# Kernel tuning notes

Hardware: AMD Instinct MI355X
Metric: run time of the kernel (lower is better)

The kernel has to match this reference:

```python
import jax, jax.numpy as jnp
import numpy as np

NORMALIZED_LENGTH = 512  # init kwarg
T_FRAMES = 32768
N_LM = 543  # mediapipe holistic landmark count


def setup_inputs() -> dict:
    key = jax.random.key(0)
    kf, kn, kd, ki = jax.random.split(key, 4)
    frames = jax.random.uniform(kf, (T_FRAMES, N_LM, 3), dtype=jnp.float32)
    nan_mask = jax.random.uniform(kn, (T_FRAMES, N_LM, 3)) < 0.10
    frames = jnp.where(nan_mask, jnp.float32(jnp.nan), frames)
    drop = jax.random.uniform(kd, (T_FRAMES,)) < 0.05
    hand_zone = jnp.arange(N_LM) >= 468
    frames = jnp.where(drop[:, None, None] & hand_zone[None, :, None], jnp.float32(jnp.nan), frames)
    lips_idx = jax.random.randint(ki, (40,), 0, 468, dtype=jnp.int32)
    return {"frames": frames, "lips_idx": lips_idx}


def _nan_mean0(x):
    # tf_nan_mean over axis 0 (keepdims); 0/0 -> NaN in TF is immediately zeroed
    # afterwards, so we emit 0 directly (identical forward values, safe grads).
    finite = ~jnp.isnan(x)
    s = jnp.where(finite, x, jnp.zeros((), x.dtype)).sum(axis=0, keepdims=True)
    c = finite.sum(axis=0, keepdims=True)
    return jnp.where(c == 0, jnp.zeros((), x.dtype), s / jnp.maximum(c, 1).astype(x.dtype))


def reference(frames, lips_idx):
    fr = frames[:, :, :2]                       # drop z coord
    lh = fr[:, 468:489]                         # [T, 21, 2]
    rh = fr[:, 522:543]                         # [T, 21, 2]
    lh = jnp.stack([lh[..., 0], 1.0 - lh[..., 1]], axis=-1)
    rh = jnp.stack([1.0 - rh[..., 0], 1.0 - rh[..., 1]], axis=-1)
    # stack hands, NaN->0, sum over the 2-hand axis
    hand = jnp.nan_to_num(lh) + jnp.nan_to_num(rh)   # [T, 21, 2]
    keep = hand.sum(axis=(1, 2)) != 0.0              # frames with >=1 visible hand
    hand = hand[keep]                                # [S, 21, 2]
    lips = fr[:, lips_idx][keep]                     # [S, 40, 2]
    lips = jnp.where(jnp.isnan(lips), _nan_mean0(lips), lips)
    raw = jnp.concatenate([hand, lips], axis=1)      # [S, 61, 2]
    S = int(raw.shape[0])
    # tf.linspace(0, S-1, L+1) cast to int32 -> segment boundaries (truncation)
    b = np.linspace(0.0, S - 1.0, NORMALIZED_LENGTH + 1).astype(np.int32)
    # frame t belongs to bin i with b[i] <= t < b[i+1]; t >= b[L] maps to L (dropped)
    seg = jnp.asarray(np.searchsorted(b, np.arange(S), side="right") - 1)
    sums = jax.ops.segment_sum(raw, seg, num_segments=NORMALIZED_LENGTH)
    cnt = jax.ops.segment_sum(jnp.ones((S,), raw.dtype), seg, num_segments=NORMALIZED_LENGTH)
    # raw is NaN-free at this point, so nan-mean == plain mean; empty bin -> NaN -> 0
    mean = jnp.where(cnt[:, None, None] == 0, jnp.zeros((), raw.dtype),
                     sums / jnp.maximum(cnt, 1.0)[:, None, None])
    sampled = mean.reshape(NORMALIZED_LENGTH, -1)    # Flatten -> [L, 122]
    rows = sampled.sum(axis=1) != 0.0                # drop all-zero (empty) bins
    return sampled[rows]
```

## Files before the change

kernel.cpp:

```cpp
#include <hip/hip_runtime.h>

#define T_FRAMES 32768
#define ROWF 1629
#define NSEG 512
#define NVAL 122
#define STRIDE 128

__global__ __launch_bounds__(256) void k1_keep_stats(
    const float* __restrict__ frames, const int* __restrict__ lips_idx,
    int* __restrict__ keep, float* __restrict__ lip_sum,
    int* __restrict__ lip_cnt, float* __restrict__ stage) {
  __shared__ float ls[80];
  __shared__ int lc[80];
  int tid = threadIdx.x;
  if (tid < 80) { ls[tid] = 0.0f; lc[tid] = 0; }
  __syncthreads();

  int lane = tid & 63;
  int wid = tid >> 6;
  int wpb = blockDim.x >> 6;
  int wpg = gridDim.x * wpb;

  for (int t = blockIdx.x * wpb + wid; t < T_FRAMES; t += wpg) {
    const float* f = frames + (size_t)t * ROWF;
    float* srow = stage + (size_t)t * STRIDE;

    float hv = 0.0f;
    if (lane < 42) {
      int j = lane >> 1, c = lane & 1;
      float lh = f[(468 + j) * 3 + c];
      float rh = f[(522 + j) * 3 + c];
      float a = (c == 0) ? lh : (1.0f - lh);
      float b = 1.0f - rh;
      a = (a == a) ? a : 0.0f;
      b = (b == b) ? b : 0.0f;
      hv = a + b;
      srow[lane] = hv;
    }
    float s = hv;
    #pragma unroll
    for (int off = 32; off > 0; off >>= 1) s += __shfl_down(s, off);
    s = __shfl(s, 0);
    int kp = (s != 0.0f) ? 1 : 0;
    if (lane == 0) keep[t] = kp;

    #pragma unroll
    for (int p = 0; p < 2; ++p) {
      int v = lane + p * 64;
      if (v < 80) {
        int j = v >> 1, c = v & 1;
        float x = f[lips_idx[j] * 3 + c];
        srow[42 + v] = x;
        if (kp && (x == x)) {
          atomicAdd(&ls[v], x);
          atomicAdd(&lc[v], 1);
        }
      }
    }
  }
  __syncthreads();
  if (tid < 80) {
    atomicAdd(&lip_sum[tid], ls[tid]);
    atomicAdd(&lip_cnt[tid], lc[tid]);
  }
}

__global__ __launch_bounds__(1024) void k2_scan(const int* __restrict__ keep,
                                                int* __restrict__ kept_t,
                                                int* __restrict__ Sp) {
  __shared__ int wsum[16];
  int tid = threadIdx.x;
  const int PER = T_FRAMES / 1024;
  int base = tid * PER;
  int fl[PER];
  int local = 0;
  #pragma unroll
  for (int k = 0; k < PER; ++k) { fl[k] = keep[base + k]; local += fl[k]; }

  int lane = tid & 63, wid = tid >> 6;
  int scan = local;
  #pragma unroll
  for (int off = 1; off < 64; off <<= 1) {
    int n = __shfl_up(scan, off);
    if (lane >= off) scan += n;
  }
  if (lane == 63) wsum[wid] = scan;
  __syncthreads();
  if (tid < 16) {
    int v = wsum[tid];
    #pragma unroll
    for (int off = 1; off < 16; off <<= 1) {
      int n = __shfl_up(v, off);
      if (tid >= off) v += n;
    }
    wsum[tid] = v;
  }
  __syncthreads();
  int excl = ((wid == 0) ? 0 : wsum[wid - 1]) + (scan - local);
  #pragma unroll
  for (int k = 0; k < PER; ++k) {
    if (fl[k]) kept_t[excl++] = base + k;
  }
  if (tid == 1023) Sp[0] = wsum[15];
}

__global__ __launch_bounds__(256) void k3_segments(
    const float* __restrict__ stage, const int* __restrict__ kept_t,
    const int* __restrict__ Sp, const float* __restrict__ lip_sum,
    const int* __restrict__ lip_cnt, float* __restrict__ out, int out_size) {
  __shared__ int seglist[128];
  __shared__ float part[NVAL];
  int tid = threadIdx.x;
  int v = tid & 127;
  int r = tid >> 7;
  int seg = blockIdx.x;
  long long Sm1 = (long long)Sp[0] - 1;
  if (Sm1 < 0) Sm1 = 0;
  int lo = (int)(((long long)seg * Sm1) >> 9);
  int hi = (int)(((long long)(seg + 1) * Sm1) >> 9);
  int cnt = hi - lo;

  for (int k = tid; k < cnt; k += 256) seglist[k] = kept_t[lo + k];
  __syncthreads();

  float cm = 0.0f;
  if (v >= 42 && v < NVAL) {
    int w = v - 42;
    int c = lip_cnt[w];
    cm = (c == 0) ? 0.0f : lip_sum[w] / (float)c;
  }

  float acc = 0.0f;
  if (v < NVAL) {
    for (int k = r; k < cnt; k += 2) {
      float x = stage[(size_t)seglist[k] * STRIDE + v];
      acc += (x == x) ? x : cm;
    }
  }
  if (r == 0 && v < NVAL) part[v] = acc;
  __syncthreads();
  if (r == 1 && v < NVAL) part[v] += acc;
  __syncthreads();
  if (r == 0 && v < NVAL) {
    float mean = (cnt == 0) ? 0.0f : part[v] / (float)cnt;
    int o = seg * NVAL + v;
    if (o < out_size) out[o] = mean;
  }
}

extern "C" void kernel_launch(void* const* d_in, const int* in_sizes, int n_in,
                              void* d_out, int out_size, void* d_ws, size_t ws_size,
                              hipStream_t stream) {
  const float* frames = (const float*)d_in[0];
  const int* lips_idx = (const int*)d_in[1];
  float* out = (float*)d_out;

  char* ws = (char*)d_ws;
  int* keep     = (int*)(ws);
  int* kept_t   = (int*)(ws + 131072);
  int* Sp       = (int*)(ws + 262144);
  float* lip_sum = (float*)(ws + 262144 + 64);
  int* lip_cnt   = (int*)(ws + 262144 + 64 + 320);
  float* stage   = (float*)(ws + 262144 + 1024);

  hipMemsetAsync(lip_sum, 0, 640, stream);

  k1_keep_stats<<<512, 256, 0, stream>>>(frames, lips_idx, keep, lip_sum,
                                         lip_cnt, stage);
  k2_scan<<<1, 1024, 0, stream>>>(keep, kept_t, Sp);
  k3_segments<<<NSEG, 256, 0, stream>>>(stage, kept_t, Sp, lip_sum, lip_cnt,
                                        out, out_size);
}
```

Measured before the change: 322.0 us.

## Use one warp per frame without grid-stride loop, pad global lip accumulators, widen segment blocks

k1 now launches 2048 blocks of 1024 threads, so each wavefront handles exactly one frame instead of grid-striding over frames. The global lip_sum/lip_cnt atomics are spread onto separate cache lines (stride 16) to reduce contention, and the memset and workspace offsets grow to match. k3 uses 512 threads with four row partitions per segment and a four-way shared reduction. The aim is more parallelism and latency hiding in the memory-bound stages. The cost is many more blocks flushing to the global atomics and larger launch overhead.

After: 320.4 us. About the same (-0.5%).

```diff
diff --git a/kernel.cpp b/kernel.cpp
--- a/kernel.cpp
+++ b/kernel.cpp
@@ -5,8 +5,9 @@
 #define NSEG 512
 #define NVAL 122
 #define STRIDE 128
+#define PADI 16
 
-__global__ __launch_bounds__(256) void k1_keep_stats(
+__global__ __launch_bounds__(1024) void k1_keep_stats(
     const float* __restrict__ frames, const int* __restrict__ lips_idx,
     int* __restrict__ keep, float* __restrict__ lip_sum,
     int* __restrict__ lip_cnt, float* __restrict__ stage) {
@@ -18,50 +19,46 @@
 
   int lane = tid & 63;
   int wid = tid >> 6;
-  int wpb = blockDim.x >> 6;
-  int wpg = gridDim.x * wpb;
+  int t = blockIdx.x * 16 + wid;
+  const float* f = frames + (size_t)t * ROWF;
+  float* srow = stage + (size_t)t * STRIDE;
 
-  for (int t = blockIdx.x * wpb + wid; t < T_FRAMES; t += wpg) {
-    const float* f = frames + (size_t)t * ROWF;
-    float* srow = stage + (size_t)t * STRIDE;
+  float hv = 0.0f;
+  if (lane < 42) {
+    int j = lane >> 1, c = lane & 1;
+    float lh = f[(468 + j) * 3 + c];
+    float rh = f[(522 + j) * 3 + c];
+    float a = (c == 0) ? lh : (1.0f - lh);
+    float b = 1.0f - rh;
+    a = (a == a) ? a : 0.0f;
+    b = (b == b) ? b : 0.0f;
+    hv = a + b;
+    srow[lane] = hv;
+  }
+  float s = hv;
+  #pragma unroll
+  for (int off = 32; off > 0; off >>= 1) s += __shfl_down(s, off);
+  s = __shfl(s, 0);
+  int kp = (s != 0.0f) ? 1 : 0;
+  if (lane == 0) keep[t] = kp;
 
-    float hv = 0.0f;
-    if (lane < 42) {
-      int j = lane >> 1, c = lane & 1;
-      float lh = f[(468 + j) * 3 + c];
-      float rh = f[(522 + j) * 3 + c];
-      float a = (c == 0) ? lh : (1.0f - lh);
-      float b = 1.0f - rh;
-      a = (a == a) ? a : 0.0f;
-      b = (b == b) ? b : 0.0f;
-      hv = a + b;
-      srow[lane] = hv;
-    }
-    float s = hv;
-    #pragma unroll
-    for (int off = 32; off > 0; off >>= 1) s += __shfl_down(s, off);
-    s = __shfl(s, 0);
-    int kp = (s != 0.0f) ? 1 : 0;
-    if (lane == 0) keep[t] = kp;
-
-    #pragma unroll
-    for (int p = 0; p < 2; ++p) {
-      int v = lane + p * 64;
-      if (v < 80) {
-        int j = v >> 1, c = v & 1;
-        float x = f[lips_idx[j] * 3 + c];
-        srow[42 + v] = x;
-        if (kp && (x == x)) {
-          atomicAdd(&ls[v], x);
-          atomicAdd(&lc[v], 1);
-        }
+  #pragma unroll
+  for (int p = 0; p < 2; ++p) {
+    int v = lane + p * 64;
+    if (v < 80) {
+      int j = v >> 1, c = v & 1;
+      float x = f[lips_idx[j] * 3 + c];
+      srow[42 + v] = x;
+      if (kp && (x == x)) {
+        atomicAdd(&ls[v], x);
+        atomicAdd(&lc[v], 1);
       }
     }
   }
   __syncthreads();
   if (tid < 80) {
-    atomicAdd(&lip_sum[tid], ls[tid]);
-    atomicAdd(&lip_cnt[tid], lc[tid]);
+    atomicAdd(&lip_sum[tid * PADI], ls[tid]);
+    atomicAdd(&lip_cnt[tid * PADI], lc[tid]);
   }
 }
 
@@ -104,12 +101,12 @@
   if (tid == 1023) Sp[0] = wsum[15];
 }
 
-__global__ __launch_bounds__(256) void k3_segments(
+__global__ __launch_bounds__(512) void k3_segments(
     const float* __restrict__ stage, const int* __restrict__ kept_t,
     const int* __restrict__ Sp, const float* __restrict__ lip_sum,
     const int* __restrict__ lip_cnt, float* __restrict__ out, int out_size) {
   __shared__ int seglist[128];
-  __shared__ float part[NVAL];
+  __shared__ float part[4][128];
   int tid = threadIdx.x;
   int v = tid & 127;
   int r = tid >> 7;
@@ -120,29 +117,28 @@
   int hi = (int)(((long long)(seg + 1) * Sm1) >> 9);
   int cnt = hi - lo;
 
-  for (int k = tid; k < cnt; k += 256) seglist[k] = kept_t[lo + k];
+  for (int k = tid; k < cnt; k += 512) seglist[k] = kept_t[lo + k];
   __syncthreads();
 
   float cm = 0.0f;
   if (v >= 42 && v < NVAL) {
     int w = v - 42;
-    int c = lip_cnt[w];
-    cm = (c == 0) ? 0.0f : lip_sum[w] / (float)c;
+    int c = lip_cnt[w * PADI];
+    cm = (c == 0) ? 0.0f : lip_sum[w * PADI] / (float)c;
   }
 
   float acc = 0.0f;
   if (v < NVAL) {
-    for (int k = r; k < cnt; k += 2) {
+    for (int k = r; k < cnt; k += 4) {
       float x = stage[(size_t)seglist[k] * STRIDE + v];
       acc += (x == x) ? x : cm;
     }
   }
-  if (r == 0 && v < NVAL) part[v] = acc;
-  __syncthreads();
-  if (r == 1 && v < NVAL) part[v] += acc;
+  part[r][v] = acc;
   __syncthreads();
   if (r == 0 && v < NVAL) {
-    float mean = (cnt == 0) ? 0.0f : part[v] / (float)cnt;
+    float tot = part[0][v] + part[1][v] + part[2][v] + part[3][v];
+    float mean = (cnt == 0) ? 0.0f : tot / (float)cnt;
     int o = seg * NVAL + v;
     if (o < out_size) out[o] = mean;
   }
@@ -156,18 +152,18 @@
   float* out = (float*)d_out;
 
   char* ws = (char*)d_ws;
-  int* keep     = (int*)(ws);
-  int* kept_t   = (int*)(ws + 131072);
-  int* Sp       = (int*)(ws + 262144);
-  float* lip_sum = (float*)(ws + 262144 + 64);
-  int* lip_cnt   = (int*)(ws + 262144 + 64 + 320);
-  float* stage   = (float*)(ws + 262144 + 1024);
+  int* keep      = (int*)(ws);
+  int* kept_t    = (int*)(ws + 131072);
+  int* Sp        = (int*)(ws + 262144);
+  float* lip_sum = (float*)(ws + 262208);
+  int* lip_cnt   = (int*)(ws + 267328);
+  float* stage   = (float*)(ws + 274432);
 
-  hipMemsetAsync(lip_sum, 0, 640, stream);
+  hipMemsetAsync((void*)lip_sum, 0, 10240, stream);
 
-  k1_keep_stats<<<512, 256, 0, stream>>>(frames, lips_idx, keep, lip_sum,
-                                         lip_cnt, stage);
+  k1_keep_stats<<<2048, 1024, 0, stream>>>(frames, lips_idx, keep, lip_sum,
+                                           lip_cnt, stage);
   k2_scan<<<1, 1024, 0, stream>>>(keep, kept_t, Sp);
-  k3_segments<<<NSEG, 256, 0, stream>>>(stage, kept_t, Sp, lip_sum, lip_cnt,
+  k3_segments<<<NSEG, 512, 0, stream>>>(stage, kept_t, Sp, lip_sum, lip_cnt,
                                         out, out_size);
 }
```
